# Kernel tuning notes

Measured on AMD Instinct MI355X. Metric: run time of the kernel, lower is better.

## Reference

```python
import jax, jax.numpy as jnp
import numpy as np

D = 1024

def setup_inputs() -> dict:
    key = jax.random.key(0)
    ks = jax.random.split(key, 9)
    s = 1.0 / np.sqrt(D)
    x = jax.random.normal(ks[0], (4096, 8, D), dtype=jnp.float32)
    Wq = jax.random.uniform(ks[1], (D, D), jnp.float32, -s, s)
    bq = jax.random.uniform(ks[2], (D,), jnp.float32, -s, s)
    Wk = jax.random.uniform(ks[3], (D, D), jnp.float32, -s, s)
    bk = jax.random.uniform(ks[4], (D,), jnp.float32, -s, s)
    Wv = jax.random.uniform(ks[5], (D, D), jnp.float32, -s, s)
    bv = jax.random.uniform(ks[6], (D,), jnp.float32, -s, s)
    Wo = jax.random.uniform(ks[7], (D, D), jnp.float32, -s, s)
    bo = jax.random.uniform(ks[8], (D,), jnp.float32, -s, s)
    return {"x": x, "Wq": Wq, "bq": bq, "Wk": Wk, "bk": bk,
            "Wv": Wv, "bv": bv, "Wo": Wo, "bo": bo}

def reference(x, Wq, bq, Wk, bk, Wv, bv, Wo, bo):
    # x: (S, B, D) seq-first, matching torch module
    Q = jax.nn.elu(x @ Wq.T + bq) + 1.0  # (S,B,D)
    K = jax.nn.elu(x @ Wk.T + bk) + 1.0  # (S,B,D)
    V = x @ Wv.T + bv                    # (S,B,D)
    # KV = K^T V per batch: (B, D, D)
    KV = jnp.einsum('sbd,sbe->bde', K, V)
    # out = Q @ KV per batch, back to (S,B,D)
    out = jnp.einsum('sbd,bde->sbe', Q, KV)
    return out @ Wo.T + bo
```

## Files before the change

### kernel.cpp

```cpp
#include <hip/hip_runtime.h>


typedef __bf16 bf16;
typedef __attribute__((ext_vector_type(8))) __bf16 bf16x8;
typedef __attribute__((ext_vector_type(4))) __bf16 bf16x4;
typedef __attribute__((ext_vector_type(4))) float f32x4;

static constexpr int S = 4096;
static constexpr int B = 8;
static constexpr int D = 1024;
static constexpr int SB = S * B;
static constexpr long long NELEM = (long long)SB * D;

__device__ __forceinline__ void load_lds16(const bf16* g, void* l)
{
    __builtin_amdgcn_global_load_lds(
        (const __attribute__((address_space(1))) void*)g,
        (__attribute__((address_space(3))) void*)l, 16, 0, 0);
}

__global__ void cvt_w3(const float* __restrict__ w0, const float* __restrict__ w1,
                       const float* __restrict__ w2, bf16* __restrict__ o0,
                       bf16* __restrict__ o1, bf16* __restrict__ o2)
{
    const float* in;
    bf16* out;
    if (blockIdx.y == 0)      { in = w0; out = o0; }
    else if (blockIdx.y == 1) { in = w1; out = o1; }
    else                      { in = w2; out = o2; }
    int i = (blockIdx.x * blockDim.x + threadIdx.x) * 4;
    float4 v = *(const float4*)(in + i);
    bf16x4 o;
    o[0] = (bf16)v.x; o[1] = (bf16)v.y; o[2] = (bf16)v.z; o[3] = (bf16)v.w;
    *(bf16x4*)(out + i) = o;
}

__global__ void cvt_permute(const float* __restrict__ in, bf16* __restrict__ out)
{
    long long i = ((long long)blockIdx.x * blockDim.x + threadIdx.x) * 8;
    const long long stride = (long long)gridDim.x * blockDim.x * 8;
    for (; i < NELEM; i += stride) {
        const long long s = i >> 13;
        const long long r = i & 8191;
        const long long b = r >> 10;
        const long long d = r & 1023;
        float4 v0 = *(const float4*)(in + i);
        float4 v1 = *(const float4*)(in + i + 4);
        bf16x8 o;
        o[0] = (bf16)v0.x; o[1] = (bf16)v0.y; o[2] = (bf16)v0.z; o[3] = (bf16)v0.w;
        o[4] = (bf16)v1.x; o[5] = (bf16)v1.y; o[6] = (bf16)v1.z; o[7] = (bf16)v1.w;
        *(bf16x8*)(out + b * ((long long)S * D) + s * D + d) = o;
    }
}

__global__ __launch_bounds__(256) void cvt_transpose_1024(
    const float* __restrict__ in, bf16* __restrict__ out)
{
    __shared__ bf16 tile[64][72];
    const int e0 = blockIdx.y * 64;
    const int d0 = blockIdx.x * 64;
    const int t  = threadIdx.x;
    const int rl = t >> 3;
    const int c8 = (t & 7) * 8;
    #pragma unroll
    for (int p = 0; p < 2; ++p) {
        int r = rl + p * 32;
        float4 v0 = *(const float4*)(in + (long long)(e0 + r) * D + d0 + c8);
        float4 v1 = *(const float4*)(in + (long long)(e0 + r) * D + d0 + c8 + 4);
        tile[c8+0][r] = (bf16)v0.x; tile[c8+1][r] = (bf16)v0.y;
        tile[c8+2][r] = (bf16)v0.z; tile[c8+3][r] = (bf16)v0.w;
        tile[c8+4][r] = (bf16)v1.x; tile[c8+5][r] = (bf16)v1.y;
        tile[c8+6][r] = (bf16)v1.z; tile[c8+7][r] = (bf16)v1.w;
    }
    __syncthreads();
    #pragma unroll
    for (int p = 0; p < 2; ++p) {
        int dr = rl + p * 32;
        *(bf16x8*)(out + (long long)(d0 + dr) * D + e0 + c8) = *(bf16x8*)(&tile[dr][c8]);
    }
}

__global__ __launch_bounds__(256) void bvo_kernel(
    const float* __restrict__ Wo, const float* __restrict__ bv, float* __restrict__ bvo)
{
    const int row = blockIdx.x;
    const int t = threadIdx.x;
    float4 w = *(const float4*)(Wo + (long long)row * D + t * 4);
    float4 b = *(const float4*)(bv + t * 4);
    float s = w.x*b.x + w.y*b.y + w.z*b.z + w.w*b.w;
    __shared__ float red[256];
    red[t] = s; __syncthreads();
    for (int off = 128; off > 0; off >>= 1) {
        if (t < off) red[t] += red[t + off];
        __syncthreads();
    }
    if (t == 0) bvo[row] = red[0];
}

__global__ __launch_bounds__(256) void kv_add(const bf16* __restrict__ p, bf16* __restrict__ o)
{
    const long long DD = (long long)D * D;
    const int b = blockIdx.y;
    const long long i = ((long long)blockIdx.x * 256 + threadIdx.x) * 8;
    bf16x8 u = *(const bf16x8*)(p + (2 * b) * DD + i);
    bf16x8 v = *(const bf16x8*)(p + (2 * b + 1) * DD + i);
    bf16x8 r;
    #pragma unroll
    for (int j = 0; j < 8; ++j) r[j] = (bf16)((float)u[j] + (float)v[j]);
    *(bf16x8*)(o + b * DD + i) = r;
}

template<int BM, int BN, int WM, int WN, int EPI, int OUTF32, int BIASROW>
__global__ __launch_bounds__(WM * WN * 64, 2) void gemm_bt(
    const bf16* __restrict__ A, const bf16* __restrict__ Bm,
    const float* __restrict__ bias, void* __restrict__ Cout,
    int lda, int ldb, int ldc, int K,
    long long aBatch, long long bBatch, long long cBatch)
{
    constexpr int THREADS = WM * WN * 64;
    constexpr int WROWS = BM / WM, WCOLS = BN / WN;
    constexpr int MI = WROWS / 16, NI = WCOLS / 16;
    constexpr int ABYTES = BM * 64;
    constexpr int BBYTES = BN * 64;
    constexpr int BUF = ABYTES + BBYTES;

    __shared__ unsigned char smem[4 * BUF];

    const int tid  = threadIdx.x;
    const int lane = tid & 63;
    const int wave = tid >> 6;
    const int wr   = wave / WN;
    const int wc   = wave % WN;
    const int bz   = blockIdx.z;

    const int nx  = gridDim.x;
    const int bid = blockIdx.y * nx + blockIdx.x;
    const int cpx = (nx * gridDim.y) >> 3;
    const int swz = (bid & 7) * cpx + (bid >> 3);
    const long long m0 = (long long)(swz / nx) * BM;
    const long long n0 = (long long)(swz % nx) * BN;

    const bf16* Ab = A  + bz * aBatch + m0 * lda;
    const bf16* Bb = Bm + bz * bBatch + n0 * ldb;

    f32x4 acc[MI][NI] = {};
    const int NT = K >> 5;

    auto stage = [&](int t) {
        unsigned char* dst = smem + (t & 3) * BUF;
        const long long kk = (long long)t << 5;
        #pragma unroll
        for (int j = 0; j < 2; ++j) {
            const int g  = wave * 64 + lane + j * THREADS;
            const int gs = g ^ ((g >> 3) & 3);
            const int row = gs >> 2, col = (gs & 3) * 8;
            load_lds16(Ab + (long long)row * lda + kk + col,
                       dst + (wave * 64 + j * THREADS) * 16);
        }
        #pragma unroll
        for (int j = 0; j < 2; ++j) {
            const int g  = wave * 64 + lane + j * THREADS;
            const int gs = g ^ ((g >> 3) & 3);
            const int row = gs >> 2, col = (gs & 3) * 8;
            load_lds16(Bb + (long long)row * ldb + kk + col,
                       dst + ABYTES + (wave * 64 + j * THREADS) * 16);
        }
    };

    stage(0); stage(1); stage(2);

    const int ko2 = (lane >> 4) * 16;
    const int la15 = lane & 15;

    for (int t = 0; t < NT; ++t) {
        if (t + 2 < NT)      asm volatile("s_waitcnt vmcnt(8)" ::: "memory");
        else if (t + 1 < NT) asm volatile("s_waitcnt vmcnt(4)" ::: "memory");
        else                 asm volatile("s_waitcnt vmcnt(0)" ::: "memory");
        __builtin_amdgcn_s_barrier();
        asm volatile("" ::: "memory");

        if (t + 3 < NT) stage(t + 3);

        const unsigned char* buf = smem + (t & 3) * BUF;
        bf16x8 a[MI], b[NI];
        #pragma unroll
        for (int mi = 0; mi < MI; ++mi) {
            int ad = (wr * WROWS + mi * 16 + la15) * 64 + ko2;
            ad ^= ((ad >> 7) & 3) << 4;
            a[mi] = *(const bf16x8*)(buf + ad);
        }
        #pragma unroll
        for (int ni = 0; ni < NI; ++ni) {
            int ad = (wc * WCOLS + ni * 16 + la15) * 64 + ko2;
            ad ^= ((ad >> 7) & 3) << 4;
            b[ni] = *(const bf16x8*)(buf + ABYTES + ad);
        }

        __builtin_amdgcn_s_setprio(1);
        #pragma unroll
        for (int mi = 0; mi < MI; ++mi)
            #pragma unroll
            for (int ni = 0; ni < NI; ++ni)
                acc[mi][ni] = __builtin_amdgcn_mfma_f32_16x16x32_bf16(
                    a[mi], b[ni], acc[mi][ni], 0, 0, 0);
        __builtin_amdgcn_s_setprio(0);
    }

    const int crow = (lane >> 4) * 4;
    const int ccol = lane & 15;
    #pragma unroll
    for (int ni = 0; ni < NI; ++ni) {
        const long long c = n0 + wc * WCOLS + ni * 16 + ccol;
        float bcol = 0.0f;
        if (!BIASROW && bias) bcol = bias[c];
        #pragma unroll
        for (int mi = 0; mi < MI; ++mi) {
            const long long r0 = m0 + wr * WROWS + mi * 16 + crow;
            #pragma unroll
            for (int j = 0; j < 4; ++j) {
                float v = acc[mi][ni][j];
                v += BIASROW ? bias[r0 + j] : bcol;
                if (EPI == 1) v = (v > 0.0f) ? (v + 1.0f) : __expf(v);
                const long long idx = bz * cBatch + (r0 + j) * ldc + c;
                if (OUTF32) ((float*)Cout)[idx] = v;
                else        ((bf16*)Cout)[idx]  = (bf16)v;
            }
        }
    }
}

template<int EPI, int OUTF32, int BIASROW, int SPLITK, int GROUPN>
__global__ __launch_bounds__(512, 1) void gemm8p(
    const bf16* __restrict__ A, const bf16* __restrict__ Bm,
    const float* __restrict__ bias, void* __restrict__ Cout,
    int lda, int ldb, int ldc, int K,
    long long aBatch, long long bBatch, long long cBatch)
{
    __shared__ unsigned char smem[131072];

    const int tid  = threadIdx.x;
    const int lane = tid & 63;
    const int wave = tid >> 6;
    const int wr   = wave >> 2;
    const int wc   = wave & 3;
    const int bz    = blockIdx.z;
    const int batch = bz / SPLITK;
    const int kseg  = bz % SPLITK;

    const int nx  = gridDim.x;
    const int ny  = gridDim.y;
    const int bid = blockIdx.y * nx + blockIdx.x;
    const int cpx = (nx * ny) >> 3;
    const int swzb = (bid & 7) * cpx + (bid >> 3);
    long long m0, n0;
    if (GROUPN) { n0 = (long long)(swzb / ny) * 256; m0 = (long long)(swzb % ny) * 256; }
    else        { m0 = (long long)(swzb / nx) * 256; n0 = (long long)(swzb % nx) * 256; }

    const bf16* Ab = A  + batch * aBatch + m0 * lda + (long long)kseg * K;
    const bf16* Bb = Bm + batch * bBatch + n0 * ldb + (long long)kseg * K;

    const int sg = (lane & 3) ^ ((lane >> 3) & 3);
    const long long srow = wave * 32 + (lane >> 2);
    const bf16* srcA  = Ab + srow * lda + sg * 8;
    const bf16* srcA2 = srcA + 16 * (long long)lda;
    const bf16* srcB  = Bb + srow * ldb + sg * 8;
    const bf16* srcB2 = srcB + 16 * (long long)ldb;
    const int dstoff = wave * 2048;

    const int la15 = lane & 15;
    const int rsw  = (lane >> 4) ^ ((la15 >> 1) & 3);
    const int a16  = (wr * 128 + la15) * 4 + rsw;
    const int b16  = (wc * 64  + la15) * 4 + rsw;

    f32x4 acc[8][4] = {};
    const int NT = K >> 6;
    const int NI = NT >> 1;

    auto stageA = [&](int T, int kh) {
        const int reg = ((((T & 1) << 1) | kh) << 14);
        const long long kp = ((long long)T << 6) + (kh << 5);
        load_lds16(srcA  + kp, smem + reg + dstoff);
        load_lds16(srcA2 + kp, smem + reg + dstoff + 1024);
    };
    auto stageB = [&](int T, int kh) {
        const int reg = 65536 + ((((T & 1) << 1) | kh) << 14);
        const long long kp = ((long long)T << 6) + (kh << 5);
        load_lds16(srcB  + kp, smem + reg + dstoff);
        load_lds16(srcB2 + kp, smem + reg + dstoff + 1024);
    };

    stageB(0, 0); stageA(0, 0); stageB(0, 1); stageA(0, 1);
    stageB(1, 0); stageA(1, 0); stageB(1, 1);
    asm volatile("s_waitcnt vmcnt(6)" ::: "memory");

    bf16x8 bfr[4];
    for (int i = 0; i < NI; ++i) {
        const int t = 2 * i;
        const bool nl = (i + 1 < NI);
        #pragma unroll
        for (int p = 0; p < 8; ++p) {
            const int ks  = (p >> 1) & 1;
            const int ch  = p & 1;
            const int buf = p >> 2;
            const int regA = ((buf << 1) | ks) << 14;
            const int regB = 65536 + regA;

            __builtin_amdgcn_s_barrier();
            __builtin_amdgcn_sched_barrier(0);

            bf16x8 afr[4];
            if (ch == 0) {
                #pragma unroll
                for (int ni = 0; ni < 4; ++ni)
                    bfr[ni] = *(const bf16x8*)(smem + regB + (b16 + ni * 64) * 16);
            }
            #pragma unroll
            for (int m4 = 0; m4 < 4; ++m4)
                afr[m4] = *(const bf16x8*)(smem + regA + (a16 + (ch * 4 + m4) * 64) * 16);

            if      (p == 0) stageA(t + 1, 1);
            else if (p == 1) { if (t + 2 < NT) stageB(t + 2, 0); }
            else if (p == 2) { if (t + 2 < NT) stageA(t + 2, 0); }
            else if (p == 3) { if (t + 2 < NT) stageB(t + 2, 1); }
            else if (p == 4) { if (t + 2 < NT) stageA(t + 2, 1); }
            else if (p == 5) { if (t + 3 < NT) stageB(t + 3, 0); }
            else if (p == 6) { if (t + 3 < NT) stageA(t + 3, 0); }
            else             { if (t + 3 < NT) stageB(t + 3, 1); }

            if (p == 3) {
                if (nl) asm volatile("s_waitcnt vmcnt(6)" ::: "memory");
                else    asm volatile("s_waitcnt vmcnt(0)" ::: "memory");
            } else if (p == 7) {
                if (nl) asm volatile("s_waitcnt vmcnt(6)" ::: "memory");
            }

            __builtin_amdgcn_s_setprio(1);
            #pragma unroll
            for (int m4 = 0; m4 < 4; ++m4)
                #pragma unroll
                for (int ni = 0; ni < 4; ++ni)
                    acc[ch * 4 + m4][ni] = __builtin_amdgcn_mfma_f32_16x16x32_bf16(
                        afr[m4], bfr[ni], acc[ch * 4 + m4][ni], 0, 0, 0);
            __builtin_amdgcn_s_setprio(0);
        }
    }

    const bool doElu = (EPI == 1) || (EPI == 2 && m0 < 1024);
    const long long cb = (long long)bz * cBatch;
    const int crow = (lane >> 4) * 4;

    if constexpr (OUTF32 != 0) {
        float* lt = (float*)smem;
        #pragma unroll
        for (int q = 0; q < 4; ++q) {
            __builtin_amdgcn_s_barrier();
            __builtin_amdgcn_sched_barrier(0);
            if (wr == (q >> 1)) {
                #pragma unroll
                for (int m4 = 0; m4 < 4; ++m4) {
                    const int mi = (q & 1) * 4 + m4;
                    const int lrow = m4 * 16 + crow;
                    const long long r0 = m0 + q * 64 + lrow;
                    #pragma unroll
                    for (int ni = 0; ni < 4; ++ni) {
                        const int lcol = wc * 64 + ni * 16 + la15;
                        float bb = 0.0f;
                        if (!BIASROW && bias) bb = bias[n0 + lcol];
                        #pragma unroll
                        for (int j = 0; j < 4; ++j) {
                            float v = acc[mi][ni][j] + (BIASROW ? bias[r0 + j] : bb);
                            if (doElu) v = (v > 0.0f) ? (v + 1.0f) : __expf(v);
                            lt[(lrow + j) * 260 + lcol] = v;
                        }
                    }
                }
            }
            __builtin_amdgcn_s_barrier();
            #pragma unroll
            for (int it = 0; it < 8; ++it) {
                const int chk = it * 512 + tid;
                const int r   = chk >> 6;
                const int g   = chk & 63;
                float4 v = *(const float4*)(lt + r * 260 + g * 4);
                *(float4*)((float*)Cout + cb + (m0 + q * 64 + r) * ldc + n0 + g * 4) = v;
            }
        }
    } else {
        bf16* lt = (bf16*)smem;
        #pragma unroll
        for (int half = 0; half < 2; ++half) {
            __builtin_amdgcn_s_barrier();
            __builtin_amdgcn_sched_barrier(0);
            if (wr == half) {
                #pragma unroll
                for (int mi = 0; mi < 8; ++mi) {
                    const int lrow = mi * 16 + crow;
                    const long long r0 = m0 + half * 128 + lrow;
                    #pragma unroll
                    for (int ni = 0; ni < 4; ++ni) {
                        const int lcol = wc * 64 + ni * 16 + la15;
                        float bb = 0.0f;
                        if (!BIASROW && bias) bb = bias[n0 + lcol];
                        #pragma unroll
                        for (int j = 0; j < 4; ++j) {
                            float v = acc[mi][ni][j] + (BIASROW ? bias[r0 + j] : bb);
                            if (doElu) v = (v > 0.0f) ? (v + 1.0f) : __expf(v);
                            lt[(lrow + j) * 264 + lcol] = (bf16)v;
                        }
                    }
                }
            }
            __builtin_amdgcn_s_barrier();
            #pragma unroll
            for (int it = 0; it < 8; ++it) {
                const int chk = it * 512 + tid;
                const int m   = chk >> 5;
                const int nof = (chk & 31) * 8;
                bf16x8 v = *(const bf16x8*)(lt + m * 264 + nof);
                *(bf16x8*)((bf16*)Cout + cb + (m0 + half * 128 + m) * ldc + n0 + nof) = v;
            }
        }
    }
}

extern "C" void kernel_launch(void* const* d_in, const int* in_sizes, int n_in,
                              void* d_out, int out_size, void* d_ws, size_t ws_size,
                              hipStream_t stream)
{
    const float* x  = (const float*)d_in[0];
    const float* Wq = (const float*)d_in[1];
    const float* bq = (const float*)d_in[2];
    const float* Wk = (const float*)d_in[3];
    const float* bk = (const float*)d_in[4];
    const float* Wv = (const float*)d_in[5];
    const float* bv = (const float*)d_in[6];
    const float* Wo = (const float*)d_in[7];
    const float* bo = (const float*)d_in[8];
    float* out = (float*)d_out;

    char* ws = (char*)d_ws;
    if (ws_size < (size_t)159383552) return;
    bf16*  xbp  = (bf16*)(ws + 0);
    bf16*  part = (bf16*)(ws + 67108864);
    bf16*  Qb   = (bf16*)(ws + 67108864);
    bf16*  wvT  = (bf16*)(ws + 134217728);
    float* bkvo = (float*)(ws + 134217728 + 2097152);
    bf16*  KVo  = (bf16*)(ws + 134217728);
    bf16*  wqb  = (bf16*)(ws + 150994944);
    bf16*  wob  = wqb + 1048576;
    bf16*  wkvo = wob + 1048576;
    bf16*  KVb  = (bf16*)d_out;

    const long long SD = (long long)S * D;

    cvt_permute<<<8192, 256, 0, stream>>>(x, xbp);
    cvt_w3<<<dim3(1024, 3), 256, 0, stream>>>(Wq, Wo, Wk, wqb, wob, wkvo);
    cvt_transpose_1024<<<dim3(16, 16), 256, 0, stream>>>(Wv, wvT);
    bvo_kernel<<<1024, 256, 0, stream>>>(Wo, bv, bkvo + 1024);
    hipMemcpyAsync(bkvo, bk, D * sizeof(float), hipMemcpyDeviceToDevice, stream);

    gemm_bt<128, 128, 2, 2, 0, 0, 0><<<dim3(8, 8, 1), 256, 0, stream>>>(
        wob, wvT, nullptr, wkvo + (long long)1024 * 1024, D, D, D, D, 0, 0, 0);

    gemm8p<2, 0, 1, 1, 1><<<dim3(16, 8, 8), 512, 0, stream>>>(
        wkvo, xbp, bkvo, KVb, D, D, S, D,
        0, SD, (long long)2048 * S);

    gemm8p<0, 0, 0, 2, 0><<<dim3(4, 4, 16), 512, 0, stream>>>(
        KVb + (long long)1024 * S, KVb, nullptr, part, S, S, D, 2048,
        (long long)2048 * S, (long long)2048 * S, (long long)D * D);

    kv_add<<<dim3(512, 8), 256, 0, stream>>>(part, KVo);

    gemm8p<1, 0, 0, 1, 0><<<dim3(4, 16, 8), 512, 0, stream>>>(
        xbp, wqb, bq, Qb, D, D, D, D, SD, 0, SD);

    gemm8p<0, 1, 0, 1, 0><<<dim3(4, 16, 8), 512, 0, stream>>>(
        Qb, KVo, bo, out, D, D, B * D, D,
        SD, (long long)D * D, (long long)D);
}
```

Measured before the change: 483.4 us.

## Compute K^T x instead of K^T V, then apply Wv·Wo projection afterwards

Instead of projecting x into both K and the combined V·Wo space (a 2048-wide GEMM over all tokens), only K is projected. KV is formed as K^T x, and the (Wo·Wv) product plus the bias term (K column sums times Wo·bv) are applied afterwards in a small per-batch D×D GEMM. This removes about half the token-level projection FLOPs. In exchange it adds an explicit bf16 transpose of x, a column-sum kernel and an extra batched GEMM, and changes where bf16 rounding happens.

Result: faster. 467.5 us (-3.3%).

```diff
diff --git a/kernel.cpp b/kernel.cpp
--- a/kernel.cpp
+++ b/kernel.cpp
@@ -53,6 +53,35 @@
     }
 }
 
+__global__ __launch_bounds__(256) void transpose_bsd_bds(
+    const bf16* __restrict__ in, bf16* __restrict__ out)
+{
+    __shared__ bf16 tile[64 * 72];
+    const int b  = blockIdx.z;
+    const int s0 = blockIdx.x * 64;
+    const int f0 = blockIdx.y * 64;
+    const int t  = threadIdx.x;
+    const int rl = t >> 3;
+    const int c8 = (t & 7) * 8;
+    const long long SD = (long long)S * D;
+
+    #pragma unroll
+    for (int p = 0; p < 2; ++p) {
+        int r = rl + p * 32;
+        bf16x8 v = *(const bf16x8*)(in + b * SD + (long long)(s0 + r) * D + f0 + c8);
+        #pragma unroll
+        for (int j = 0; j < 8; ++j)
+            tile[(c8 + j) * 72 + r] = v[j];
+    }
+    __syncthreads();
+    #pragma unroll
+    for (int p = 0; p < 2; ++p) {
+        int fr = rl + p * 32;
+        *(bf16x8*)(out + b * SD + (long long)(f0 + fr) * S + s0 + c8) =
+            *(const bf16x8*)(&tile[fr * 72 + c8]);
+    }
+}
+
 __global__ __launch_bounds__(256) void cvt_transpose_1024(
     const float* __restrict__ in, bf16* __restrict__ out)
 {
@@ -97,7 +126,25 @@
     if (t == 0) bvo[row] = red[0];
 }
 
-__global__ __launch_bounds__(256) void kv_add(const bf16* __restrict__ p, bf16* __restrict__ o)
+__global__ __launch_bounds__(256) void kcolsum(const bf16* __restrict__ Kt,
+                                               float* __restrict__ ks)
+{
+    const int row  = blockIdx.x * 4 + (threadIdx.x >> 6);
+    const int lane = threadIdx.x & 63;
+    const bf16* r = Kt + (long long)row * S;
+    float s = 0.0f;
+    #pragma unroll
+    for (int it = 0; it < 8; ++it) {
+        bf16x8 v = *(const bf16x8*)(r + it * 512 + lane * 8);
+        #pragma unroll
+        for (int j = 0; j < 8; ++j) s += (float)v[j];
+    }
+    #pragma unroll
+    for (int off = 32; off > 0; off >>= 1) s += __shfl_down(s, off);
+    if (lane == 0) ks[row] = s;
+}
+
+__global__ __launch_bounds__(256) void kv_add(bf16* __restrict__ p)
 {
     const long long DD = (long long)D * D;
     const int b = blockIdx.y;
@@ -107,7 +154,7 @@
     bf16x8 r;
     #pragma unroll
     for (int j = 0; j < 8; ++j) r[j] = (bf16)((float)u[j] + (float)v[j]);
-    *(bf16x8*)(o + b * DD + i) = r;
+    *(bf16x8*)(p + (2 * b) * DD + i) = r;
 }
 
 template<int BM, int BN, int WM, int WN, int EPI, int OUTF32, int BIASROW>
@@ -232,7 +279,8 @@
 template<int EPI, int OUTF32, int BIASROW, int SPLITK, int GROUPN>
 __global__ __launch_bounds__(512, 1) void gemm8p(
     const bf16* __restrict__ A, const bf16* __restrict__ Bm,
-    const float* __restrict__ bias, void* __restrict__ Cout,
+    const float* __restrict__ bias, const float* __restrict__ ksum,
+    void* __restrict__ Cout,
     int lda, int ldb, int ldc, int K,
     long long aBatch, long long bBatch, long long cBatch)
 {
@@ -401,10 +449,18 @@
                         const int lcol = wc * 64 + ni * 16 + la15;
                         float bb = 0.0f;
                         if (!BIASROW && bias) bb = bias[n0 + lcol];
+                        float ksv = 0.0f;
+                        if (EPI == 3 && ksum)
+                            ksv = ksum[(long long)batch * D + n0 + lcol];
                         #pragma unroll
                         for (int j = 0; j < 4; ++j) {
-                            float v = acc[mi][ni][j] + (BIASROW ? bias[r0 + j] : bb);
-                            if (doElu) v = (v > 0.0f) ? (v + 1.0f) : __expf(v);
+                            float v;
+                            if (EPI == 3) {
+                                v = acc[mi][ni][j] + bias[r0 + j] * ksv;
+                            } else {
+                                v = acc[mi][ni][j] + (BIASROW ? bias[r0 + j] : bb);
+                                if (doElu) v = (v > 0.0f) ? (v + 1.0f) : __expf(v);
+                            }
                             lt[(lrow + j) * 264 + lcol] = (bf16)v;
                         }
                     }
@@ -443,39 +499,46 @@
     bf16*  xbp  = (bf16*)(ws + 0);
     bf16*  part = (bf16*)(ws + 67108864);
     bf16*  Qb   = (bf16*)(ws + 67108864);
+    float* ks   = (float*)(ws + 100663296);
+    float* bvo  = (float*)(ws + 100663296 + 32768);
     bf16*  wvT  = (bf16*)(ws + 134217728);
-    float* bkvo = (float*)(ws + 134217728 + 2097152);
     bf16*  KVo  = (bf16*)(ws + 134217728);
     bf16*  wqb  = (bf16*)(ws + 150994944);
     bf16*  wob  = wqb + 1048576;
-    bf16*  wkvo = wob + 1048576;
-    bf16*  KVb  = (bf16*)d_out;
+    bf16*  wkb  = wob + 1048576;
+    bf16*  Wvo  = wkb + 1048576;
+    bf16*  Kt   = (bf16*)d_out;
+    bf16*  xT   = Kt + NELEM;
 
     const long long SD = (long long)S * D;
+    const long long DD = (long long)D * D;
 
     cvt_permute<<<8192, 256, 0, stream>>>(x, xbp);
-    cvt_w3<<<dim3(1024, 3), 256, 0, stream>>>(Wq, Wo, Wk, wqb, wob, wkvo);
+    cvt_w3<<<dim3(1024, 3), 256, 0, stream>>>(Wq, Wo, Wk, wqb, wob, wkb);
     cvt_transpose_1024<<<dim3(16, 16), 256, 0, stream>>>(Wv, wvT);
-    bvo_kernel<<<1024, 256, 0, stream>>>(Wo, bv, bkvo + 1024);
-    hipMemcpyAsync(bkvo, bk, D * sizeof(float), hipMemcpyDeviceToDevice, stream);
+    bvo_kernel<<<1024, 256, 0, stream>>>(Wo, bv, bvo);
+    transpose_bsd_bds<<<dim3(64, 16, 8), 256, 0, stream>>>(xbp, xT);
 
     gemm_bt<128, 128, 2, 2, 0, 0, 0><<<dim3(8, 8, 1), 256, 0, stream>>>(
-        wob, wvT, nullptr, wkvo + (long long)1024 * 1024, D, D, D, D, 0, 0, 0);
-
-    gemm8p<2, 0, 1, 1, 1><<<dim3(16, 8, 8), 512, 0, stream>>>(
-        wkvo, xbp, bkvo, KVb, D, D, S, D,
-        0, SD, (long long)2048 * S);
+        wob, wvT, nullptr, Wvo, D, D, D, D, 0, 0, 0);
+
+    gemm8p<1, 0, 1, 1, 1><<<dim3(16, 4, 8), 512, 0, stream>>>(
+        wkb, xbp, bk, nullptr, Kt, D, D, S, D, 0, SD, SD);
+
+    kcolsum<<<2048, 256, 0, stream>>>(Kt, ks);
 
     gemm8p<0, 0, 0, 2, 0><<<dim3(4, 4, 16), 512, 0, stream>>>(
-        KVb + (long long)1024 * S, KVb, nullptr, part, S, S, D, 2048,
-        (long long)2048 * S, (long long)2048 * S, (long long)D * D);
-
-    kv_add<<<dim3(512, 8), 256, 0, stream>>>(part, KVo);
+        Kt, xT, nullptr, nullptr, part, S, S, D, 2048, SD, SD, DD);
+
+    kv_add<<<dim3(512, 8), 256, 0, stream>>>(part);
+
+    gemm8p<3, 0, 1, 1, 0><<<dim3(4, 4, 8), 512, 0, stream>>>(
+        Wvo, part, bvo, ks, KVo, D, D, D, D, 0, 2 * DD, DD);
 
     gemm8p<1, 0, 0, 1, 0><<<dim3(4, 16, 8), 512, 0, stream>>>(
-        xbp, wqb, bq, Qb, D, D, D, D, SD, 0, SD);
+        xbp, wqb, bq, nullptr, Qb, D, D, D, D, SD, 0, SD);
 
     gemm8p<0, 1, 0, 1, 0><<<dim3(4, 16, 8), 512, 0, stream>>>(
-        Qb, KVo, bo, out, D, D, B * D, D,
-        SD, (long long)D * D, (long long)D);
-}
+        Qb, KVo, bo, nullptr, out, D, D, B * D, D,
+        SD, DD, (long long)D);
+}
```
